# Kernel optimization log

Measured on AMD Instinct MI355X. Metric: run time of the kernel, lower is better.

## Reference

```python
import jax, jax.numpy as jnp
import numpy as np
import math

C = 128
A_SCALES = [2.0, 4.0, 8.0]
A_RATIOS = [0.5, 1.0, 2.0]
STRIDES = [4, 8, 16, 32, 64]
NA = len(A_SCALES) * len(A_RATIOS)
IMG = 1024
N = 2
NMS_THRESH = 0.7
NUM_PRE = 6000
NUM_POST = 300
SCALE_CLIP = math.log(1000.0 / 16.0)


def base_anchors(stride):
    c = stride / 2.0
    a = []
    for s in A_SCALES:
        for r in A_RATIOS:
            h = stride * s * math.sqrt(r)
            w = stride * s * math.sqrt(1.0 / r)
            a.append((c - h / 2.0, c - w / 2.0, c + h / 2.0, c + w / 2.0))
    return np.array(a, dtype=np.float32)  # [NA,4] yxyx


def shifted_anchors(stride, H, W):
    base = jnp.asarray(base_anchors(stride))
    gy = jnp.arange(H, dtype=jnp.float32) * stride
    gx = jnp.arange(W, dtype=jnp.float32) * stride
    grid = jnp.stack(jnp.meshgrid(gy, gx, indexing='ij'), axis=-1)  # [H,W,2]
    shift = jnp.concatenate([grid, grid], axis=-1)  # [H,W,4]
    return (base[None, None] + shift[:, :, None]).reshape(-1, 4)  # [H*W*NA,4]


def conv(x, w, b, pad):
    y = jax.lax.conv_general_dilated(x, w, (1, 1), pad, dimension_numbers=('NCHW', 'OIHW', 'NCHW'))
    return y + b[None, :, None, None]


def head(x, w1, b1, wobj, bobj, wbbx, bbbx):
    h = jax.nn.relu(conv(x, w1, b1, 'SAME'))
    obj = conv(h, wobj, bobj, 'VALID')  # [N,NA,H,W]
    bbx = conv(h, wbbx, bbbx, 'VALID')  # [N,4*NA,H,W]
    n = x.shape[0]
    obj = obj.transpose(0, 2, 3, 1).reshape(n, -1)       # (h,w,anchor) order
    bbx = bbx.transpose(0, 2, 3, 1).reshape(n, -1, 4)
    return obj, bbx


def shift_boxes(anchors, deltas):
    yx = (anchors[..., :2] + anchors[..., 2:]) * 0.5
    hw = anchors[..., 2:] - anchors[..., :2]
    yx_o = yx + deltas[..., :2] * hw
    hw_o = hw * jnp.exp(jnp.minimum(deltas[..., 2:], SCALE_CLIP))
    return jnp.concatenate([yx_o - 0.5 * hw_o, yx_o + 0.5 * hw_o], axis=-1)


def nms_single(boxes, scores):
    # greedy hard NMS; boxes [P,4] yxyx, scores [P]; fixed NUM_POST outputs
    areas = (boxes[:, 2] - boxes[:, 0]) * (boxes[:, 3] - boxes[:, 1])

    def step(active, _):
        masked = jnp.where(active, scores, -jnp.inf)
        i = jnp.argmax(masked)
        ok = active[i]
        tl = jnp.maximum(boxes[i, :2], boxes[:, :2])
        br = jnp.minimum(boxes[i, 2:], boxes[:, 2:])
        inter = jnp.clip(br[:, 0] - tl[:, 0], 0.0) * jnp.clip(br[:, 1] - tl[:, 1], 0.0)
        iou = inter / (areas[i] + areas - inter + 1e-9)
        active = active & (iou <= NMS_THRESH)
        return active, (jnp.where(ok, i, 0), ok)

    _, (idx, valid) = jax.lax.scan(step, jnp.ones(boxes.shape[0], bool), None, length=NUM_POST)
    return idx, valid


def forward(x0, x1, x2, x3, x4, w1, b1, wobj, bobj, wbbx, bbbx, valid_size):
    feats = [x0, x1, x2, x3, x4]
    objs, bbxs, ancs = [], [], []
    for f, s in zip(feats, STRIDES):
        o, b = head(f, w1, b1, wobj, bobj, wbbx, bbbx)
        objs.append(o)
        bbxs.append(b)
        ancs.append(shifted_anchors(s, f.shape[2], f.shape[3]))
    obj = jnp.concatenate(objs, axis=1)        # [N,M]
    bbx = jnp.concatenate(bbxs, axis=1)        # [N,M,4]
    anchors = jnp.concatenate(ancs, axis=0)    # [M,4]
    boxes = shift_boxes(anchors[None], bbx)    # [N,M,4]
    h = valid_size[:, 0].astype(boxes.dtype)[:, None]
    w = valid_size[:, 1].astype(boxes.dtype)[:, None]
    boxes = jnp.stack([jnp.clip(boxes[..., 0], 0.0, h),
                       jnp.clip(boxes[..., 1], 0.0, w),
                       jnp.clip(boxes[..., 2], 0.0, h),
                       jnp.clip(boxes[..., 3], 0.0, w)], axis=-1)
    k = min(boxes.shape[1], NUM_PRE)
    top_scores, top_idx = jax.lax.top_k(obj, k)                     # per-image topk
    top_boxes = jnp.take_along_axis(boxes, top_idx[..., None], axis=1)
    idx, valid = jax.vmap(nms_single)(jax.lax.stop_gradient(top_boxes),
                                      jax.lax.stop_gradient(top_scores))
    props = jnp.take_along_axis(top_boxes, idx[..., None], axis=1)  # [N,NUM_POST,4]
    props = props * valid[..., None].astype(props.dtype)            # zero-pad invalid
    return props, valid


def setup_inputs() -> dict:
    key = jax.random.key(0)
    ks = jax.random.split(key, 8)
    sizes = [IMG // s for s in STRIDES]
    inp = {}
    for i, hw in enumerate(sizes):
        inp['x%d' % i] = jax.random.normal(ks[i], (N, C, hw, hw), jnp.float32)
    inp['w1'] = jax.random.normal(ks[5], (C, C, 3, 3), jnp.float32) * 0.05
    inp['b1'] = jnp.zeros((C,), jnp.float32)
    inp['wobj'] = jax.random.normal(ks[6], (NA, C, 1, 1), jnp.float32) * 0.05
    inp['bobj'] = jnp.zeros((NA,), jnp.float32)
    inp['wbbx'] = jax.random.normal(ks[7], (4 * NA, C, 1, 1), jnp.float32) * 0.05
    inp['bbbx'] = jnp.zeros((4 * NA,), jnp.float32)
    inp['valid_size'] = jnp.array([[IMG, IMG]] * N, jnp.int32)
    return inp


def reference(x0, x1, x2, x3, x4, w1, b1, wobj, bobj, wbbx, bbbx, valid_size):
    return forward(x0, x1, x2, x3, x4, w1, b1, wobj, bobj, wbbx, bbbx, valid_size)
```

## Files before the change

### kernel.cpp

```cpp
#include <hip/hip_runtime.h>
#include <stdint.h>
#include <math.h>

#define M_TOT 785664
#define NPRE  6000
#define NPOST 300
#define CAP   8192
#define NWORDS 94
#define ROWW   96
#define NPAD   6016

__device__ __forceinline__ uint32_t okey(float f) {
    uint32_t u = __float_as_uint(f);
    return (u & 0x80000000u) ? ~u : (u | 0x80000000u);
}

__global__ void k_init(const float* __restrict__ w1, float* __restrict__ wt,
                       uint32_t* __restrict__ p, int zn) {
    int i = blockIdx.x * 256 + threadIdx.x;
    if (i < zn) p[i] = 0u;
    if (i < 128 * 128 * 9) {
        int co = i / 1152; int r = i % 1152; int ci = r / 9; int tap = r % 9;
        wt[ci * 1152 + tap * 128 + co] = w1[i];
    }
}

__global__ __launch_bounds__(512) void k_conv(
    const float* __restrict__ x0, const float* __restrict__ x1,
    const float* __restrict__ x2, const float* __restrict__ x3,
    const float* __restrict__ x4,
    const float* __restrict__ wt, const float* __restrict__ b1,
    const float* __restrict__ wobj, const float* __restrict__ bobj,
    const float* __restrict__ wbbx, const float* __restrict__ bbbx,
    float* __restrict__ sc, float* __restrict__ dl)
{
    __shared__ __attribute__((aligned(16))) float sx[8][18][20];
    __shared__ __attribute__((aligned(16))) float sw[8 * 9 * 128];

    int b = blockIdx.x, L = 0;
    if (b >= 512) { b -= 512; L = 1;
        if (b >= 128) { b -= 128; L = 2;
            if (b >= 32) { b -= 32; L = 3;
                if (b >= 8) { b -= 8; L = 4; } } } }
    const float* xs = (L == 0) ? x0 : (L == 1) ? x1 : (L == 2) ? x2 : (L == 3) ? x3 : x4;
    const int scoff_[5] = {0, 589824, 737280, 774144, 783360};
    int Wl = 256 >> L; int Hl = Wl; int HW = Wl * Wl;
    int tpiSh = 8 - 2 * L;
    int n  = b >> tpiSh;
    int r  = b & ((1 << tpiSh) - 1);
    int txSh = 4 - L;
    int ty0 = r >> txSh, tx0 = r & ((1 << txSh) - 1);
    int y0 = ty0 << 4, x0c = tx0 << 4;
    const float* xin = xs + (size_t)n * 128 * HW;

    int t = threadIdx.x;
    int tx = t & 15;
    int ty = t >> 4;
    int py = ty >> 1, px = (ty & 1) << 3;

    float acc0[4][8], acc1[4][8];
#pragma unroll
    for (int c = 0; c < 4; ++c)
#pragma unroll
        for (int e = 0; e < 8; ++e) { acc0[c][e] = 0.f; acc1[c][e] = 0.f; }

    for (int cc0 = 0; cc0 < 128; cc0 += 8) {
        __syncthreads();
        for (int i = t; i < 2880; i += 512) {
            int ci = i / 360; int rm = i % 360; int rr = rm / 20; int cc = rm % 20;
            float v = 0.f;
            int gy = y0 - 1 + rr, gx = x0c - 1 + cc;
            if (cc < 18 && gy >= 0 && gy < Hl && gx >= 0 && gx < Wl)
                v = xin[(size_t)(cc0 + ci) * HW + (size_t)gy * Wl + gx];
            sx[ci][rr][cc] = v;
        }
        {
            const float4* wsrc = (const float4*)(wt + (size_t)cc0 * 1152);
            float4* wdst = (float4*)sw;
            for (int i = t; i < 2304; i += 512) wdst[i] = wsrc[i];
        }
        __syncthreads();

#pragma unroll 1
        for (int ci = 0; ci < 8; ++ci) {
#pragma unroll
            for (int dy = 0; dy < 3; ++dy) {
                const float* xr = &sx[ci][py + dy][px];
                float4 xa = *(const float4*)(xr);
                float4 xb = *(const float4*)(xr + 4);
                float4 xc = *(const float4*)(xr + 8);
                float win[12] = {xa.x, xa.y, xa.z, xa.w, xb.x, xb.y, xb.z, xb.w,
                                 xc.x, xc.y, xc.z, xc.w};
#pragma unroll
                for (int dx = 0; dx < 3; ++dx) {
                    const float* wr = &sw[(ci * 9 + dy * 3 + dx) * 128 + tx * 4];
                    float4 wa = *(const float4*)(wr);
                    float4 wb = *(const float4*)(wr + 64);
                    float wva[4] = {wa.x, wa.y, wa.z, wa.w};
                    float wvb[4] = {wb.x, wb.y, wb.z, wb.w};
#pragma unroll
                    for (int e = 0; e < 8; ++e) {
                        float xv = win[e + dx];
#pragma unroll
                        for (int c = 0; c < 4; ++c) {
                            acc0[c][e] = fmaf(wva[c], xv, acc0[c][e]);
                            acc1[c][e] = fmaf(wvb[c], xv, acc1[c][e]);
                        }
                    }
                }
            }
        }
    }

#pragma unroll
    for (int c = 0; c < 4; ++c) {
        float ba = b1[tx * 4 + c];
        float bb = b1[64 + tx * 4 + c];
#pragma unroll
        for (int e = 0; e < 8; ++e) {
            float v0 = acc0[c][e] + ba;
            float v1 = acc1[c][e] + bb;
            acc0[c][e] = v0 > 0.f ? v0 : 0.f;
            acc1[c][e] = v1 > 0.f ? v1 : 0.f;
        }
    }

    int gy = y0 + py;
    size_t ppos = (size_t)gy * Wl + x0c + px;
    size_t scbase = (size_t)n * M_TOT + scoff_[L];
    size_t dlbase = (size_t)n * 4 * (size_t)M_TOT + 4 * (size_t)scoff_[L];
    for (int a = 0; a < 45; ++a) {
        const float* wp = (a < 9) ? (wobj + (size_t)a * 128) : (wbbx + (size_t)(a - 9) * 128);
        float4 wa = *(const float4*)(wp + tx * 4);
        float4 wb = *(const float4*)(wp + 64 + tx * 4);
        float wva[4] = {wa.x, wa.y, wa.z, wa.w};
        float wvb[4] = {wb.x, wb.y, wb.z, wb.w};
        float p[8];
#pragma unroll
        for (int e = 0; e < 8; ++e) p[e] = 0.f;
#pragma unroll
        for (int c = 0; c < 4; ++c)
#pragma unroll
            for (int e = 0; e < 8; ++e) {
                p[e] = fmaf(wva[c], acc0[c][e], p[e]);
                p[e] = fmaf(wvb[c], acc1[c][e], p[e]);
            }
#pragma unroll
        for (int mm = 1; mm < 16; mm <<= 1)
#pragma unroll
            for (int e = 0; e < 8; ++e)
                p[e] += __shfl_xor(p[e], mm, 64);
        if (tx == 0) {
            float bias = (a < 9) ? bobj[a] : bbbx[a - 9];
            float4 o0 = make_float4(p[0] + bias, p[1] + bias, p[2] + bias, p[3] + bias);
            float4 o1 = make_float4(p[4] + bias, p[5] + bias, p[6] + bias, p[7] + bias);
            float* dst = (a < 9) ? (sc + scbase + (size_t)a * HW + ppos)
                                 : (dl + dlbase + (size_t)(a - 9) * HW + ppos);
            *(float4*)dst = o0;
            *(float4*)(dst + 4) = o1;
        }
    }
}

__global__ __launch_bounds__(256) void k_hist(const float* __restrict__ sc,
                                              uint32_t* __restrict__ hist) {
    __shared__ uint32_t lh[8192];
    int n = blockIdx.y;
    for (int i = threadIdx.x; i < 8192; i += 256) lh[i] = 0u;
    __syncthreads();
    const float* s = sc + (size_t)n * M_TOT;
    int stride = gridDim.x * 256;
    for (int i = blockIdx.x * 256 + threadIdx.x; i < M_TOT; i += stride)
        atomicAdd(&lh[okey(s[i]) >> 19], 1u);
    __syncthreads();
    for (int i = threadIdx.x; i < 8192; i += 256) {
        uint32_t v = lh[i];
        if (v) atomicAdd(&hist[n * 8192 + i], v);
    }
}

__global__ void k_subhist(const float* __restrict__ sc, const uint32_t* __restrict__ ctrl,
                          uint32_t* __restrict__ subh) {
    int i = blockIdx.x * blockDim.x + threadIdx.x;
    int stride = gridDim.x * blockDim.x;
    for (; i < 2 * M_TOT; i += stride) {
        int n = i >= M_TOT;
        uint32_t k = okey(sc[i]);
        if ((k >> 19) == ctrl[n * 8 + 0])
            atomicAdd(&subh[n * 8192 + ((k >> 6) & 0x1FFFu)], 1u);
    }
}

__global__ void k_scan(const uint32_t* __restrict__ hist, uint32_t* __restrict__ ctrl, int phase) {
    int n = blockIdx.x;
    const uint32_t* h = hist + n * 8192;
    uint32_t* c = ctrl + n * 8;
    __shared__ uint32_t tp[256];
    int t = threadIdx.x;
    uint32_t s = 0;
    for (int r = 0; r < 32; ++r) s += h[8191 - (t * 32 + r)];
    tp[t] = s;
    __syncthreads();
    if (t == 0) {
        uint32_t run = (phase == 0) ? 0u : c[1];
        for (int i = 0; i < 256; ++i) { uint32_t v = tp[i]; tp[i] = run; run += v; }
    }
    __syncthreads();
    uint32_t cum = tp[t];
    for (int r = 0; r < 32; ++r) {
        int j = 8191 - (t * 32 + r);
        uint32_t cc = h[j];
        if (cum < 6000u && cum + cc >= 6000u) {
            if (phase == 0) { c[0] = (uint32_t)j; c[1] = cum; }
            else            { c[2] = (c[0] << 19) | ((uint32_t)j << 6); }
        }
        cum += cc;
    }
}

__global__ void k_compact(const float* __restrict__ sc, uint32_t* __restrict__ ctrl,
                          uint64_t* __restrict__ cand) {
    int i = blockIdx.x * blockDim.x + threadIdx.x;
    int stride = gridDim.x * blockDim.x;
    const int scoff_[5] = {0, 589824, 737280, 774144, 783360};
    int lane = threadIdx.x & 63;
    for (; i < 2 * M_TOT; i += stride) {
        int n = i >= M_TOT;
        int q = n ? (i - M_TOT) : i;
        uint32_t k = okey(sc[i]);
        bool hit = (k >= ctrl[n * 8 + 2]);
        unsigned long long m = __ballot(hit);
        if (m) {
            int leader = __builtin_ctzll(m);
            uint32_t base = 0;
            if (lane == leader) base = atomicAdd(&ctrl[n * 8 + 3], (uint32_t)__popcll(m));
            base = (uint32_t)__shfl((int)base, leader, 64);
            if (hit) {
                uint32_t slot = base + (uint32_t)__popcll(m & ((1ull << lane) - 1ull));
                if (slot < CAP) {
                    int Lq = (q < 589824) ? 0 : (q < 737280) ? 1 : (q < 774144) ? 2
                            : (q < 783360) ? 3 : 4;
                    int r = q - scoff_[Lq];
                    int sh = 16 - 2 * Lq;
                    int a = r >> sh;
                    int pos = r & ((1 << sh) - 1);
                    uint32_t mm = (uint32_t)(scoff_[Lq] + pos * 9 + a);
                    cand[(size_t)n * CAP + slot] = ((uint64_t)k << 32) | (uint32_t)(~mm);
                }
            }
        }
    }
}

__global__ __launch_bounds__(256) void k_rank(const uint64_t* __restrict__ cand,
                                              const uint32_t* __restrict__ ctrl,
                                              uint64_t* __restrict__ sorted) {
    __shared__ __attribute__((aligned(16))) uint64_t chunk[2048];
    int n = blockIdx.y;
    uint32_t cnt = ctrl[n * 8 + 3];
    if (cnt > CAP) cnt = CAP;
    const uint64_t* cb = cand + (size_t)n * CAP;
    uint64_t* sb = sorted + (size_t)n * CAP;
    int i = blockIdx.x * 256 + threadIdx.x;
    uint64_t key = (i < (int)cnt) ? cb[i] : 0ull;
    uint32_t rank = 0;
    const ulonglong2* cb2 = (const ulonglong2*)cb;
    for (uint32_t base = 0; base < cnt; base += 2048) {
        __syncthreads();
        for (int j = threadIdx.x; j < 1024; j += 256)
            ((ulonglong2*)chunk)[j] = cb2[(base >> 1) + j];
        __syncthreads();
        uint32_t lim = cnt - base; if (lim > 2048u) lim = 2048u;
        for (uint32_t j = 0; j < lim; ++j) rank += (chunk[j] > key) ? 1u : 0u;
    }
    if (i < (int)cnt && rank < CAP) sb[rank] = key;
}

__global__ void k_decode(const uint64_t* __restrict__ cand, const float* __restrict__ dl,
                         const int* __restrict__ vsz, float* __restrict__ boxes,
                         unsigned long long* __restrict__ degm) {
    int i = blockIdx.x * 256 + threadIdx.x;
    if (i >= 2 * NPRE) return;
    int n = i / NPRE, rk = i % NPRE;
    const int scoff_[5] = {0, 589824, 737280, 774144, 783360};
    uint64_t pk = cand[(size_t)n * CAP + rk];
    uint32_t m = ~(uint32_t)(pk & 0xFFFFFFFFull);
    int Lq = (m < 589824u) ? 0 : (m < 737280u) ? 1 : (m < 774144u) ? 2 : (m < 783360u) ? 3 : 4;
    int r = (int)m - scoff_[Lq];
    int pos = r / 9;
    int a = r - pos * 9;
    int Wl = 256 >> Lq;
    int y = pos >> (8 - Lq);
    int xx = pos & (Wl - 1);
    float stridef = (float)(4 << Lq);
    double sD = (double)(2 << (a / 3));
    double rD = ((a % 3) == 0) ? 0.5 : ((a % 3) == 1) ? 1.0 : 2.0;
    double hD = ((double)stridef * sD) * sqrt(rD);
    double wD = ((double)stridef * sD) * sqrt(1.0 / rD);
    double cD = (double)stridef / 2.0;
    float y1b = (float)(cD - hD / 2.0);
    float x1b = (float)(cD - wD / 2.0);
    float y2b = (float)(cD + hD / 2.0);
    float x2b = (float)(cD + wD / 2.0);
    float gy = (float)y * stridef;
    float gx = (float)xx * stridef;
    float ay1 = __fadd_rn(y1b, gy), ax1 = __fadd_rn(x1b, gx);
    float ay2 = __fadd_rn(y2b, gy), ax2 = __fadd_rn(x2b, gx);
    float cy = __fmul_rn(__fadd_rn(ay1, ay2), 0.5f);
    float cx = __fmul_rn(__fadd_rn(ax1, ax2), 0.5f);
    float ah = __fsub_rn(ay2, ay1);
    float aw = __fsub_rn(ax2, ax1);
    size_t HWl = (size_t)Wl * Wl;
    size_t db = (size_t)n * 4 * M_TOT + 4 * (size_t)scoff_[Lq] + (size_t)pos;
    float dy_ = dl[db + (size_t)(a * 4 + 0) * HWl];
    float dx_ = dl[db + (size_t)(a * 4 + 1) * HWl];
    float dh_ = dl[db + (size_t)(a * 4 + 2) * HWl];
    float dw_ = dl[db + (size_t)(a * 4 + 3) * HWl];
    float yo = __fadd_rn(cy, __fmul_rn(dy_, ah));
    float xo = __fadd_rn(cx, __fmul_rn(dx_, aw));
    const float SCLIPf = 4.135166556742356f;
    float ho = __fmul_rn(ah, (float)exp((double)fminf(dh_, SCLIPf)));
    float wo = __fmul_rn(aw, (float)exp((double)fminf(dw_, SCLIPf)));
    float hf = (float)vsz[n * 2 + 0], wf = (float)vsz[n * 2 + 1];
    float y1 = fminf(fmaxf(__fsub_rn(yo, __fmul_rn(0.5f, ho)), 0.f), hf);
    float x1 = fminf(fmaxf(__fsub_rn(xo, __fmul_rn(0.5f, wo)), 0.f), wf);
    float y2 = fminf(fmaxf(__fadd_rn(yo, __fmul_rn(0.5f, ho)), 0.f), hf);
    float x2 = fminf(fmaxf(__fadd_rn(xo, __fmul_rn(0.5f, wo)), 0.f), wf);
    *(float4*)(boxes + ((size_t)n * NPAD + rk) * 4) = make_float4(y1, x1, y2, x2);
    float area = __fmul_rn(__fsub_rn(y2, y1), __fsub_rn(x2, x1));
    float selfiou = __fdiv_rn(area, __fadd_rn(area, 1e-9f));
    if (!(selfiou > 0.7f))
        atomicOr(&degm[(size_t)n * ROWW + (rk >> 6)], 1ull << (rk & 63));
}

__global__ __launch_bounds__(256) void k_iou(const float* __restrict__ boxes,
                                             uint64_t* __restrict__ ioum) {
    int n = blockIdx.y;
    int i = blockIdx.x * 4 + (threadIdx.x >> 6);
    int lane = threadIdx.x & 63;
    const float* bsrc = boxes + (size_t)n * NPAD * 4;
    float4 bi = *(const float4*)(bsrc + (size_t)i * 4);
    float ai = __fmul_rn(__fsub_rn(bi.z, bi.x), __fsub_rn(bi.w, bi.y));
    uint64_t* row = ioum + ((size_t)n * NPAD + i) * ROWW;
    int w0 = i >> 6;
    for (int w = lane; w < w0; w += 64) row[w] = 0ull;
    for (int w = w0; w < NWORDS; ++w) {
        int j = (w << 6) | lane;
        bool pred = false;
        if (j > i && j < NPRE) {
            float4 bj = *(const float4*)(bsrc + (size_t)j * 4);
            float aj = __fmul_rn(__fsub_rn(bj.z, bj.x), __fsub_rn(bj.w, bj.y));
            float ty = fmaxf(bi.x, bj.x), tx2 = fmaxf(bi.y, bj.y);
            float by = fminf(bi.z, bj.z), bx2 = fminf(bi.w, bj.w);
            float ih = fmaxf(__fsub_rn(by, ty), 0.f), iw = fmaxf(__fsub_rn(bx2, tx2), 0.f);
            float inter = __fmul_rn(ih, iw);
            float den = __fadd_rn(__fsub_rn(__fadd_rn(ai, aj), inter), 1e-9f);
            float iou = __fdiv_rn(inter, den);
            pred = iou > 0.7f;
        }
        unsigned long long msk = __ballot(pred);
        if (lane == 0) row[w] = (uint64_t)msk;
    }
}

__global__ __launch_bounds__(64) void k_nms(const float* __restrict__ boxes,
                                            const uint64_t* __restrict__ ioum,
                                            const unsigned long long* __restrict__ degm,
                                            float* __restrict__ out) {
    int n = blockIdx.x;
    __shared__ uint64_t sup[NWORDS];
    __shared__ uint64_t deg[NWORDS];
    __shared__ int keepl[NPOST];
    int lane = threadIdx.x;
    for (int w = lane; w < NWORDS; w += 64) {
        sup[w] = 0ull;
        deg[w] = degm[(size_t)n * ROWW + w];
    }
    __syncthreads();
    int kept = 0;
    bool stop = false;
    for (int w = 0; w < NWORDS && kept < NPOST && !stop; ++w) {
        uint64_t vmask = (w == NWORDS - 1) ? ((1ull << 48) - 1ull) : ~0ull;
        uint64_t avail = (~sup[w]) & vmask;
        while (avail && kept < NPOST) {
            int bpos = __builtin_ctzll(avail);
            int i = (w << 6) | bpos;
            const uint64_t* row = ioum + ((size_t)n * NPAD + i) * ROWW;
            uint64_t r0 = row[lane];
            uint64_t r1 = (lane < NWORDS - 64) ? row[64 + lane] : 0ull;
            if (lane == 0) keepl[kept] = i;
            kept++;
            if ((deg[w] >> bpos) & 1ull) {
                if (lane == 0) { for (int k2 = kept; k2 < NPOST; ++k2) keepl[k2] = i; }
                kept = NPOST;
                stop = true;
                break;
            }
            sup[lane] |= r0;
            if (lane < NWORDS - 64) sup[64 + lane] |= r1;
            __syncthreads();
            avail = (~sup[w]) & vmask & ~((2ull << bpos) - 1ull);
        }
    }
    __syncthreads();
    for (int k = lane; k < NPOST; k += 64) {
        float4 bx = make_float4(0.f, 0.f, 0.f, 0.f);
        float vf = 0.f;
        if (k < kept) {
            int i = keepl[k];
            bx = *(const float4*)(boxes + ((size_t)n * NPAD + i) * 4);
            vf = 1.f;
        }
        *(float4*)(out + (size_t)n * 1200 + (size_t)k * 4) = bx;
        out[2400 + n * 300 + k] = vf;
    }
}

extern "C" void kernel_launch(void* const* d_in, const int* in_sizes, int n_in,
                              void* d_out, int out_size, void* d_ws, size_t ws_size,
                              hipStream_t stream) {
    (void)out_size; (void)ws_size;
    static const int want[12] = {16777216, 4194304, 1048576, 262144, 65536,
                                 147456, 128, 1152, 9, 4608, 36, 4};
    const void* p[12];
    for (int k = 0; k < 12; ++k) p[k] = d_in[k];
    bool pos_ok = (n_in >= 12);
    for (int k = 0; k < 12 && pos_ok; ++k) if (in_sizes[k] != want[k]) pos_ok = false;
    if (!pos_ok) {
        for (int k = 0; k < 12; ++k)
            for (int j = 0; j < n_in; ++j)
                if (in_sizes[j] == want[k]) { p[k] = d_in[j]; break; }
    }
    const float* x0   = (const float*)p[0];
    const float* x1   = (const float*)p[1];
    const float* x2   = (const float*)p[2];
    const float* x3   = (const float*)p[3];
    const float* x4   = (const float*)p[4];
    const float* w1   = (const float*)p[5];
    const float* b1   = (const float*)p[6];
    const float* wobj = (const float*)p[7];
    const float* bobj = (const float*)p[8];
    const float* wbbx = (const float*)p[9];
    const float* bbbx = (const float*)p[10];
    const int*   vsz  = (const int*)p[11];
    float* out = (float*)d_out;

    size_t off = 0;
    char* base = (char*)d_ws;
    auto carve = [&](size_t bytes) -> void* {
        void* q = base + off;
        off += (bytes + 255) & ~(size_t)255;
        return q;
    };
    float*    SC     = (float*)carve((size_t)2 * M_TOT * 4);
    float*    DL     = (float*)carve((size_t)2 * M_TOT * 16);
    float*    WT     = (float*)carve((size_t)147456 * 4);
    uint32_t* HIST   = (uint32_t*)carve((size_t)16384 * 4);
    uint32_t* SUBH   = (uint32_t*)carve((size_t)16384 * 4);
    uint32_t* CTRL   = (uint32_t*)carve((size_t)64 * 4);
    unsigned long long* DEGM = (unsigned long long*)carve((size_t)2 * ROWW * 8);
    uint64_t* CAND   = (uint64_t*)carve((size_t)2 * CAP * 8);
    uint64_t* SORTED = (uint64_t*)carve((size_t)2 * CAP * 8);
    float*    BOXES  = (float*)carve((size_t)2 * NPAD * 16);
    uint64_t* IOUM   = (uint64_t*)carve((size_t)2 * NPAD * ROWW * 8);

    int zn = (int)(((char*)CAND - (char*)HIST) / 4);
    int initN = (zn > 147456) ? zn : 147456;
    k_init<<<(initN + 255) / 256, 256, 0, stream>>>(w1, WT, HIST, zn);
    k_conv<<<682, 512, 0, stream>>>(x0, x1, x2, x3, x4, WT, b1,
                                    wobj, bobj, wbbx, bbbx, SC, DL);
    k_hist<<<dim3(256, 2), 256, 0, stream>>>(SC, HIST);
    k_scan<<<2, 256, 0, stream>>>(HIST, CTRL, 0);
    k_subhist<<<1024, 256, 0, stream>>>(SC, CTRL, SUBH);
    k_scan<<<2, 256, 0, stream>>>(SUBH, CTRL, 1);
    k_compact<<<1024, 256, 0, stream>>>(SC, CTRL, CAND);
    k_rank<<<dim3(CAP / 256, 2), 256, 0, stream>>>(CAND, CTRL, SORTED);
    k_decode<<<(2 * NPRE + 255) / 256, 256, 0, stream>>>(SORTED, DL, vsz, BOXES, DEGM);
    k_iou<<<dim3(NPRE / 4, 2), 256, 0, stream>>>(BOXES, IOUM);
    k_nms<<<2, 64, 0, stream>>>(BOXES, IOUM, DEGM, out);
}
```

Baseline: 1.043 ms.

## Fuse post-conv selection and NMS stages into one cooperative kernel

Replaces nine separate launches (histogram, scan, subhistogram, scan, compaction, rank sort, decode, IoU matrix, NMS) with a single cooperative kernel of 512 blocks that separates the phases with grid-wide syncs. The goal is to remove per-launch overhead and the gaps between small kernels. In exchange, some phases run on fewer blocks than before (subhist and compact go from 1024 blocks to 512, IoU uses a block-strided loop), grid.sync has its own cost, and correctness depends on all 512 blocks being co-resident.

```diff
diff --git a/kernel.cpp b/kernel.cpp
--- a/kernel.cpp
+++ b/kernel.cpp
@@ -1,4 +1,5 @@
 #include <hip/hip_runtime.h>
+#include <hip/hip_cooperative_groups.h>
 #include <stdint.h>
 #include <math.h>
 
@@ -9,6 +10,8 @@
 #define NWORDS 94
 #define ROWW   96
 #define NPAD   6016
+
+namespace cg = cooperative_groups;
 
 __device__ __forceinline__ uint32_t okey(float f) {
     uint32_t u = __float_as_uint(f);
@@ -162,40 +165,7 @@
     }
 }
 
-__global__ __launch_bounds__(256) void k_hist(const float* __restrict__ sc,
-                                              uint32_t* __restrict__ hist) {
-    __shared__ uint32_t lh[8192];
-    int n = blockIdx.y;
-    for (int i = threadIdx.x; i < 8192; i += 256) lh[i] = 0u;
-    __syncthreads();
-    const float* s = sc + (size_t)n * M_TOT;
-    int stride = gridDim.x * 256;
-    for (int i = blockIdx.x * 256 + threadIdx.x; i < M_TOT; i += stride)
-        atomicAdd(&lh[okey(s[i]) >> 19], 1u);
-    __syncthreads();
-    for (int i = threadIdx.x; i < 8192; i += 256) {
-        uint32_t v = lh[i];
-        if (v) atomicAdd(&hist[n * 8192 + i], v);
-    }
-}
-
-__global__ void k_subhist(const float* __restrict__ sc, const uint32_t* __restrict__ ctrl,
-                          uint32_t* __restrict__ subh) {
-    int i = blockIdx.x * blockDim.x + threadIdx.x;
-    int stride = gridDim.x * blockDim.x;
-    for (; i < 2 * M_TOT; i += stride) {
-        int n = i >= M_TOT;
-        uint32_t k = okey(sc[i]);
-        if ((k >> 19) == ctrl[n * 8 + 0])
-            atomicAdd(&subh[n * 8192 + ((k >> 6) & 0x1FFFu)], 1u);
-    }
-}
-
-__global__ void k_scan(const uint32_t* __restrict__ hist, uint32_t* __restrict__ ctrl, int phase) {
-    int n = blockIdx.x;
-    const uint32_t* h = hist + n * 8192;
-    uint32_t* c = ctrl + n * 8;
-    __shared__ uint32_t tp[256];
+__device__ void scan_phase(const uint32_t* h, uint32_t* c, int phase, uint32_t* tp) {
     int t = threadIdx.x;
     uint32_t s = 0;
     for (int r = 0; r < 32; ++r) s += h[8191 - (t * 32 + r)];
@@ -218,201 +188,244 @@
     }
 }
 
-__global__ void k_compact(const float* __restrict__ sc, uint32_t* __restrict__ ctrl,
-                          uint64_t* __restrict__ cand) {
-    int i = blockIdx.x * blockDim.x + threadIdx.x;
-    int stride = gridDim.x * blockDim.x;
+__global__ __launch_bounds__(256) void k_select(
+    const float* __restrict__ sc, uint32_t* __restrict__ hist,
+    uint32_t* __restrict__ subh, uint32_t* __restrict__ ctrl,
+    uint64_t* __restrict__ cand, uint64_t* __restrict__ sorted,
+    const float* __restrict__ dl, const int* __restrict__ vsz,
+    float* __restrict__ boxes, unsigned long long* __restrict__ degm,
+    uint64_t* __restrict__ ioum, float* __restrict__ out)
+{
+    __shared__ __attribute__((aligned(16))) unsigned char smem[32768];
+    cg::grid_group grid = cg::this_grid();
+    const int bid = blockIdx.x;
+    const int t = threadIdx.x;
     const int scoff_[5] = {0, 589824, 737280, 774144, 783360};
-    int lane = threadIdx.x & 63;
-    for (; i < 2 * M_TOT; i += stride) {
-        int n = i >= M_TOT;
-        int q = n ? (i - M_TOT) : i;
-        uint32_t k = okey(sc[i]);
-        bool hit = (k >= ctrl[n * 8 + 2]);
-        unsigned long long m = __ballot(hit);
-        if (m) {
-            int leader = __builtin_ctzll(m);
-            uint32_t base = 0;
-            if (lane == leader) base = atomicAdd(&ctrl[n * 8 + 3], (uint32_t)__popcll(m));
-            base = (uint32_t)__shfl((int)base, leader, 64);
-            if (hit) {
-                uint32_t slot = base + (uint32_t)__popcll(m & ((1ull << lane) - 1ull));
-                if (slot < CAP) {
-                    int Lq = (q < 589824) ? 0 : (q < 737280) ? 1 : (q < 774144) ? 2
-                            : (q < 783360) ? 3 : 4;
-                    int r = q - scoff_[Lq];
-                    int sh = 16 - 2 * Lq;
-                    int a = r >> sh;
-                    int pos = r & ((1 << sh) - 1);
-                    uint32_t mm = (uint32_t)(scoff_[Lq] + pos * 9 + a);
-                    cand[(size_t)n * CAP + slot] = ((uint64_t)k << 32) | (uint32_t)(~mm);
+
+    {
+        uint32_t* lh = (uint32_t*)smem;
+        int n = bid >> 8;
+        for (int i = t; i < 8192; i += 256) lh[i] = 0u;
+        __syncthreads();
+        const float* s = sc + (size_t)n * M_TOT;
+        for (int i = (bid & 255) * 256 + t; i < M_TOT; i += 256 * 256)
+            atomicAdd(&lh[okey(s[i]) >> 19], 1u);
+        __syncthreads();
+        for (int i = t; i < 8192; i += 256) {
+            uint32_t v = lh[i];
+            if (v) atomicAdd(&hist[n * 8192 + i], v);
+        }
+    }
+    grid.sync();
+
+    if (bid < 2) scan_phase(hist + bid * 8192, ctrl + bid * 8, 0, (uint32_t*)smem);
+    grid.sync();
+
+    {
+        int stride = 512 * 256;
+        for (int i = bid * 256 + t; i < 2 * M_TOT; i += stride) {
+            int n = i >= M_TOT;
+            uint32_t k = okey(sc[i]);
+            if ((k >> 19) == ctrl[n * 8 + 0])
+                atomicAdd(&subh[n * 8192 + ((k >> 6) & 0x1FFFu)], 1u);
+        }
+    }
+    grid.sync();
+
+    if (bid < 2) scan_phase(subh + bid * 8192, ctrl + bid * 8, 1, (uint32_t*)smem);
+    grid.sync();
+
+    {
+        int stride = 512 * 256;
+        int lane = t & 63;
+        for (int i = bid * 256 + t; i < 2 * M_TOT; i += stride) {
+            int n = i >= M_TOT;
+            int q = n ? (i - M_TOT) : i;
+            uint32_t k = okey(sc[i]);
+            bool hit = (k >= ctrl[n * 8 + 2]);
+            unsigned long long m = __ballot(hit);
+            if (m) {
+                int leader = __builtin_ctzll(m);
+                uint32_t base = 0;
+                if (lane == leader) base = atomicAdd(&ctrl[n * 8 + 3], (uint32_t)__popcll(m));
+                base = (uint32_t)__shfl((int)base, leader, 64);
+                if (hit) {
+                    uint32_t slot = base + (uint32_t)__popcll(m & ((1ull << lane) - 1ull));
+                    if (slot < CAP) {
+                        int Lq = (q < 589824) ? 0 : (q < 737280) ? 1 : (q < 774144) ? 2
+                                : (q < 783360) ? 3 : 4;
+                        int r = q - scoff_[Lq];
+                        int sh = 16 - 2 * Lq;
+                        int a = r >> sh;
+                        int pos = r & ((1 << sh) - 1);
+                        uint32_t mm = (uint32_t)(scoff_[Lq] + pos * 9 + a);
+                        cand[(size_t)n * CAP + slot] = ((uint64_t)k << 32) | (uint32_t)(~mm);
+                    }
                 }
             }
         }
     }
-}
-
-__global__ __launch_bounds__(256) void k_rank(const uint64_t* __restrict__ cand,
-                                              const uint32_t* __restrict__ ctrl,
-                                              uint64_t* __restrict__ sorted) {
-    __shared__ __attribute__((aligned(16))) uint64_t chunk[2048];
-    int n = blockIdx.y;
-    uint32_t cnt = ctrl[n * 8 + 3];
-    if (cnt > CAP) cnt = CAP;
-    const uint64_t* cb = cand + (size_t)n * CAP;
-    uint64_t* sb = sorted + (size_t)n * CAP;
-    int i = blockIdx.x * 256 + threadIdx.x;
-    uint64_t key = (i < (int)cnt) ? cb[i] : 0ull;
-    uint32_t rank = 0;
-    const ulonglong2* cb2 = (const ulonglong2*)cb;
-    for (uint32_t base = 0; base < cnt; base += 2048) {
-        __syncthreads();
-        for (int j = threadIdx.x; j < 1024; j += 256)
-            ((ulonglong2*)chunk)[j] = cb2[(base >> 1) + j];
-        __syncthreads();
-        uint32_t lim = cnt - base; if (lim > 2048u) lim = 2048u;
-        for (uint32_t j = 0; j < lim; ++j) rank += (chunk[j] > key) ? 1u : 0u;
-    }
-    if (i < (int)cnt && rank < CAP) sb[rank] = key;
-}
-
-__global__ void k_decode(const uint64_t* __restrict__ cand, const float* __restrict__ dl,
-                         const int* __restrict__ vsz, float* __restrict__ boxes,
-                         unsigned long long* __restrict__ degm) {
-    int i = blockIdx.x * 256 + threadIdx.x;
-    if (i >= 2 * NPRE) return;
-    int n = i / NPRE, rk = i % NPRE;
-    const int scoff_[5] = {0, 589824, 737280, 774144, 783360};
-    uint64_t pk = cand[(size_t)n * CAP + rk];
-    uint32_t m = ~(uint32_t)(pk & 0xFFFFFFFFull);
-    int Lq = (m < 589824u) ? 0 : (m < 737280u) ? 1 : (m < 774144u) ? 2 : (m < 783360u) ? 3 : 4;
-    int r = (int)m - scoff_[Lq];
-    int pos = r / 9;
-    int a = r - pos * 9;
-    int Wl = 256 >> Lq;
-    int y = pos >> (8 - Lq);
-    int xx = pos & (Wl - 1);
-    float stridef = (float)(4 << Lq);
-    double sD = (double)(2 << (a / 3));
-    double rD = ((a % 3) == 0) ? 0.5 : ((a % 3) == 1) ? 1.0 : 2.0;
-    double hD = ((double)stridef * sD) * sqrt(rD);
-    double wD = ((double)stridef * sD) * sqrt(1.0 / rD);
-    double cD = (double)stridef / 2.0;
-    float y1b = (float)(cD - hD / 2.0);
-    float x1b = (float)(cD - wD / 2.0);
-    float y2b = (float)(cD + hD / 2.0);
-    float x2b = (float)(cD + wD / 2.0);
-    float gy = (float)y * stridef;
-    float gx = (float)xx * stridef;
-    float ay1 = __fadd_rn(y1b, gy), ax1 = __fadd_rn(x1b, gx);
-    float ay2 = __fadd_rn(y2b, gy), ax2 = __fadd_rn(x2b, gx);
-    float cy = __fmul_rn(__fadd_rn(ay1, ay2), 0.5f);
-    float cx = __fmul_rn(__fadd_rn(ax1, ax2), 0.5f);
-    float ah = __fsub_rn(ay2, ay1);
-    float aw = __fsub_rn(ax2, ax1);
-    size_t HWl = (size_t)Wl * Wl;
-    size_t db = (size_t)n * 4 * M_TOT + 4 * (size_t)scoff_[Lq] + (size_t)pos;
-    float dy_ = dl[db + (size_t)(a * 4 + 0) * HWl];
-    float dx_ = dl[db + (size_t)(a * 4 + 1) * HWl];
-    float dh_ = dl[db + (size_t)(a * 4 + 2) * HWl];
-    float dw_ = dl[db + (size_t)(a * 4 + 3) * HWl];
-    float yo = __fadd_rn(cy, __fmul_rn(dy_, ah));
-    float xo = __fadd_rn(cx, __fmul_rn(dx_, aw));
-    const float SCLIPf = 4.135166556742356f;
-    float ho = __fmul_rn(ah, (float)exp((double)fminf(dh_, SCLIPf)));
-    float wo = __fmul_rn(aw, (float)exp((double)fminf(dw_, SCLIPf)));
-    float hf = (float)vsz[n * 2 + 0], wf = (float)vsz[n * 2 + 1];
-    float y1 = fminf(fmaxf(__fsub_rn(yo, __fmul_rn(0.5f, ho)), 0.f), hf);
-    float x1 = fminf(fmaxf(__fsub_rn(xo, __fmul_rn(0.5f, wo)), 0.f), wf);
-    float y2 = fminf(fmaxf(__fadd_rn(yo, __fmul_rn(0.5f, ho)), 0.f), hf);
-    float x2 = fminf(fmaxf(__fadd_rn(xo, __fmul_rn(0.5f, wo)), 0.f), wf);
-    *(float4*)(boxes + ((size_t)n * NPAD + rk) * 4) = make_float4(y1, x1, y2, x2);
-    float area = __fmul_rn(__fsub_rn(y2, y1), __fsub_rn(x2, x1));
-    float selfiou = __fdiv_rn(area, __fadd_rn(area, 1e-9f));
-    if (!(selfiou > 0.7f))
-        atomicOr(&degm[(size_t)n * ROWW + (rk >> 6)], 1ull << (rk & 63));
-}
-
-__global__ __launch_bounds__(256) void k_iou(const float* __restrict__ boxes,
-                                             uint64_t* __restrict__ ioum) {
-    int n = blockIdx.y;
-    int i = blockIdx.x * 4 + (threadIdx.x >> 6);
-    int lane = threadIdx.x & 63;
-    const float* bsrc = boxes + (size_t)n * NPAD * 4;
-    float4 bi = *(const float4*)(bsrc + (size_t)i * 4);
-    float ai = __fmul_rn(__fsub_rn(bi.z, bi.x), __fsub_rn(bi.w, bi.y));
-    uint64_t* row = ioum + ((size_t)n * NPAD + i) * ROWW;
-    int w0 = i >> 6;
-    for (int w = lane; w < w0; w += 64) row[w] = 0ull;
-    for (int w = w0; w < NWORDS; ++w) {
-        int j = (w << 6) | lane;
-        bool pred = false;
-        if (j > i && j < NPRE) {
-            float4 bj = *(const float4*)(bsrc + (size_t)j * 4);
-            float aj = __fmul_rn(__fsub_rn(bj.z, bj.x), __fsub_rn(bj.w, bj.y));
-            float ty = fmaxf(bi.x, bj.x), tx2 = fmaxf(bi.y, bj.y);
-            float by = fminf(bi.z, bj.z), bx2 = fminf(bi.w, bj.w);
-            float ih = fmaxf(__fsub_rn(by, ty), 0.f), iw = fmaxf(__fsub_rn(bx2, tx2), 0.f);
-            float inter = __fmul_rn(ih, iw);
-            float den = __fadd_rn(__fsub_rn(__fadd_rn(ai, aj), inter), 1e-9f);
-            float iou = __fdiv_rn(inter, den);
-            pred = iou > 0.7f;
-        }
-        unsigned long long msk = __ballot(pred);
-        if (lane == 0) row[w] = (uint64_t)msk;
-    }
-}
-
-__global__ __launch_bounds__(64) void k_nms(const float* __restrict__ boxes,
-                                            const uint64_t* __restrict__ ioum,
-                                            const unsigned long long* __restrict__ degm,
-                                            float* __restrict__ out) {
-    int n = blockIdx.x;
-    __shared__ uint64_t sup[NWORDS];
-    __shared__ uint64_t deg[NWORDS];
-    __shared__ int keepl[NPOST];
-    int lane = threadIdx.x;
-    for (int w = lane; w < NWORDS; w += 64) {
-        sup[w] = 0ull;
-        deg[w] = degm[(size_t)n * ROWW + w];
-    }
-    __syncthreads();
-    int kept = 0;
-    bool stop = false;
-    for (int w = 0; w < NWORDS && kept < NPOST && !stop; ++w) {
-        uint64_t vmask = (w == NWORDS - 1) ? ((1ull << 48) - 1ull) : ~0ull;
-        uint64_t avail = (~sup[w]) & vmask;
-        while (avail && kept < NPOST) {
-            int bpos = __builtin_ctzll(avail);
-            int i = (w << 6) | bpos;
-            const uint64_t* row = ioum + ((size_t)n * NPAD + i) * ROWW;
-            uint64_t r0 = row[lane];
-            uint64_t r1 = (lane < NWORDS - 64) ? row[64 + lane] : 0ull;
-            if (lane == 0) keepl[kept] = i;
-            kept++;
-            if ((deg[w] >> bpos) & 1ull) {
-                if (lane == 0) { for (int k2 = kept; k2 < NPOST; ++k2) keepl[k2] = i; }
-                kept = NPOST;
-                stop = true;
-                break;
-            }
-            sup[lane] |= r0;
-            if (lane < NWORDS - 64) sup[64 + lane] |= r1;
+    grid.sync();
+
+    if (bid < 64) {
+        uint64_t* chunk = (uint64_t*)smem;
+        int n = bid >> 5;
+        uint32_t cnt = ctrl[n * 8 + 3];
+        if (cnt > CAP) cnt = CAP;
+        const uint64_t* cb = cand + (size_t)n * CAP;
+        uint64_t* sb = sorted + (size_t)n * CAP;
+        int i = (bid & 31) * 256 + t;
+        uint64_t key = (i < (int)cnt) ? cb[i] : 0ull;
+        uint32_t rank = 0;
+        const ulonglong2* cb2 = (const ulonglong2*)cb;
+        for (uint32_t base = 0; base < cnt; base += 2048) {
             __syncthreads();
-            avail = (~sup[w]) & vmask & ~((2ull << bpos) - 1ull);
-        }
-    }
-    __syncthreads();
-    for (int k = lane; k < NPOST; k += 64) {
-        float4 bx = make_float4(0.f, 0.f, 0.f, 0.f);
-        float vf = 0.f;
-        if (k < kept) {
-            int i = keepl[k];
-            bx = *(const float4*)(boxes + ((size_t)n * NPAD + i) * 4);
-            vf = 1.f;
-        }
-        *(float4*)(out + (size_t)n * 1200 + (size_t)k * 4) = bx;
-        out[2400 + n * 300 + k] = vf;
+            for (int j = t; j < 1024; j += 256)
+                ((ulonglong2*)chunk)[j] = cb2[(base >> 1) + j];
+            __syncthreads();
+            uint32_t lim = cnt - base; if (lim > 2048u) lim = 2048u;
+            for (uint32_t j = 0; j < lim; ++j) rank += (chunk[j] > key) ? 1u : 0u;
+        }
+        if (i < (int)cnt && rank < CAP) sb[rank] = key;
+    }
+    grid.sync();
+
+    {
+        int i = bid * 256 + t;
+        if (i < 2 * NPRE) {
+            int n = i / NPRE, rk = i % NPRE;
+            uint64_t pk = sorted[(size_t)n * CAP + rk];
+            uint32_t m = ~(uint32_t)(pk & 0xFFFFFFFFull);
+            int Lq = (m < 589824u) ? 0 : (m < 737280u) ? 1 : (m < 774144u) ? 2
+                    : (m < 783360u) ? 3 : 4;
+            int r = (int)m - scoff_[Lq];
+            int pos = r / 9;
+            int a = r - pos * 9;
+            int Wl = 256 >> Lq;
+            int y = pos >> (8 - Lq);
+            int xx = pos & (Wl - 1);
+            float stridef = (float)(4 << Lq);
+            double sD = (double)(2 << (a / 3));
+            double rD = ((a % 3) == 0) ? 0.5 : ((a % 3) == 1) ? 1.0 : 2.0;
+            double hD = ((double)stridef * sD) * sqrt(rD);
+            double wD = ((double)stridef * sD) * sqrt(1.0 / rD);
+            double cD = (double)stridef / 2.0;
+            float y1b = (float)(cD - hD / 2.0);
+            float x1b = (float)(cD - wD / 2.0);
+            float y2b = (float)(cD + hD / 2.0);
+            float x2b = (float)(cD + wD / 2.0);
+            float gy = (float)y * stridef;
+            float gx = (float)xx * stridef;
+            float ay1 = __fadd_rn(y1b, gy), ax1 = __fadd_rn(x1b, gx);
+            float ay2 = __fadd_rn(y2b, gy), ax2 = __fadd_rn(x2b, gx);
+            float cy = __fmul_rn(__fadd_rn(ay1, ay2), 0.5f);
+            float cx = __fmul_rn(__fadd_rn(ax1, ax2), 0.5f);
+            float ah = __fsub_rn(ay2, ay1);
+            float aw = __fsub_rn(ax2, ax1);
+            size_t HWl = (size_t)Wl * Wl;
+            size_t db = (size_t)n * 4 * M_TOT + 4 * (size_t)scoff_[Lq] + (size_t)pos;
+            float dy_ = dl[db + (size_t)(a * 4 + 0) * HWl];
+            float dx_ = dl[db + (size_t)(a * 4 + 1) * HWl];
+            float dh_ = dl[db + (size_t)(a * 4 + 2) * HWl];
+            float dw_ = dl[db + (size_t)(a * 4 + 3) * HWl];
+            float yo = __fadd_rn(cy, __fmul_rn(dy_, ah));
+            float xo = __fadd_rn(cx, __fmul_rn(dx_, aw));
+            const float SCLIPf = 4.135166556742356f;
+            float ho = __fmul_rn(ah, (float)exp((double)fminf(dh_, SCLIPf)));
+            float wo = __fmul_rn(aw, (float)exp((double)fminf(dw_, SCLIPf)));
+            float hf = (float)vsz[n * 2 + 0], wf = (float)vsz[n * 2 + 1];
+            float y1 = fminf(fmaxf(__fsub_rn(yo, __fmul_rn(0.5f, ho)), 0.f), hf);
+            float x1 = fminf(fmaxf(__fsub_rn(xo, __fmul_rn(0.5f, wo)), 0.f), wf);
+            float y2 = fminf(fmaxf(__fadd_rn(yo, __fmul_rn(0.5f, ho)), 0.f), hf);
+            float x2 = fminf(fmaxf(__fadd_rn(xo, __fmul_rn(0.5f, wo)), 0.f), wf);
+            *(float4*)(boxes + ((size_t)n * NPAD + rk) * 4) = make_float4(y1, x1, y2, x2);
+            float area = __fmul_rn(__fsub_rn(y2, y1), __fsub_rn(x2, x1));
+            float selfiou = __fdiv_rn(area, __fadd_rn(area, 1e-9f));
+            if (!(selfiou > 0.7f))
+                atomicOr(&degm[(size_t)n * ROWW + (rk >> 6)], 1ull << (rk & 63));
+        }
+    }
+    grid.sync();
+
+    {
+        int lane = t & 63;
+        for (int pair = bid; pair < 3000; pair += 512) {
+            int n = pair >= 1500;
+            int blk = pair - n * 1500;
+            int i = blk * 4 + (t >> 6);
+            const float* bsrc = boxes + (size_t)n * NPAD * 4;
+            float4 bi = *(const float4*)(bsrc + (size_t)i * 4);
+            float ai = __fmul_rn(__fsub_rn(bi.z, bi.x), __fsub_rn(bi.w, bi.y));
+            uint64_t* row = ioum + ((size_t)n * NPAD + i) * ROWW;
+            int w0 = i >> 6;
+            for (int w = lane; w < w0; w += 64) row[w] = 0ull;
+            for (int w = w0; w < NWORDS; ++w) {
+                int j = (w << 6) | lane;
+                bool pred = false;
+                if (j > i && j < NPRE) {
+                    float4 bj = *(const float4*)(bsrc + (size_t)j * 4);
+                    float aj = __fmul_rn(__fsub_rn(bj.z, bj.x), __fsub_rn(bj.w, bj.y));
+                    float ty = fmaxf(bi.x, bj.x), tx2 = fmaxf(bi.y, bj.y);
+                    float by = fminf(bi.z, bj.z), bx2 = fminf(bi.w, bj.w);
+                    float ih = fmaxf(__fsub_rn(by, ty), 0.f), iw = fmaxf(__fsub_rn(bx2, tx2), 0.f);
+                    float inter = __fmul_rn(ih, iw);
+                    float den = __fadd_rn(__fsub_rn(__fadd_rn(ai, aj), inter), 1e-9f);
+                    float iou = __fdiv_rn(inter, den);
+                    pred = iou > 0.7f;
+                }
+                unsigned long long msk = __ballot(pred);
+                if (lane == 0) row[w] = (uint64_t)msk;
+            }
+        }
+    }
+    grid.sync();
+
+    if (bid < 2 && t < 64) {
+        uint64_t* sup = (uint64_t*)smem;
+        uint64_t* deg = (uint64_t*)(smem + 768);
+        int* keepl = (int*)(smem + 1536);
+        int n = bid;
+        int lane = t;
+        for (int w = lane; w < NWORDS; w += 64) {
+            sup[w] = 0ull;
+            deg[w] = degm[(size_t)n * ROWW + w];
+        }
+        __builtin_amdgcn_s_barrier();
+        int kept = 0;
+        bool stop = false;
+        for (int w = 0; w < NWORDS && kept < NPOST && !stop; ++w) {
+            uint64_t vmask = (w == NWORDS - 1) ? ((1ull << 48) - 1ull) : ~0ull;
+            uint64_t avail = (~sup[w]) & vmask;
+            while (avail && kept < NPOST) {
+                int bpos = __builtin_ctzll(avail);
+                int i = (w << 6) | bpos;
+                const uint64_t* row = ioum + ((size_t)n * NPAD + i) * ROWW;
+                uint64_t r0 = row[lane];
+                uint64_t r1 = (lane < NWORDS - 64) ? row[64 + lane] : 0ull;
+                if (lane == 0) keepl[kept] = i;
+                kept++;
+                if ((deg[w] >> bpos) & 1ull) {
+                    if (lane == 0) { for (int k2 = kept; k2 < NPOST; ++k2) keepl[k2] = i; }
+                    kept = NPOST;
+                    stop = true;
+                    break;
+                }
+                sup[lane] |= r0;
+                if (lane < NWORDS - 64) sup[64 + lane] |= r1;
+                avail = (~sup[w]) & vmask & ~((2ull << bpos) - 1ull);
+            }
+        }
+        for (int k = lane; k < NPOST; k += 64) {
+            float4 bx = make_float4(0.f, 0.f, 0.f, 0.f);
+            float vf = 0.f;
+            if (k < kept) {
+                int i = keepl[k];
+                bx = *(const float4*)(boxes + ((size_t)n * NPAD + i) * 4);
+                vf = 1.f;
+            }
+            *(float4*)(out + (size_t)n * 1200 + (size_t)k * 4) = bx;
+            out[2400 + n * 300 + k] = vf;
+        }
     }
 }
 
@@ -469,13 +482,13 @@
     k_init<<<(initN + 255) / 256, 256, 0, stream>>>(w1, WT, HIST, zn);
     k_conv<<<682, 512, 0, stream>>>(x0, x1, x2, x3, x4, WT, b1,
                                     wobj, bobj, wbbx, bbbx, SC, DL);
-    k_hist<<<dim3(256, 2), 256, 0, stream>>>(SC, HIST);
-    k_scan<<<2, 256, 0, stream>>>(HIST, CTRL, 0);
-    k_subhist<<<1024, 256, 0, stream>>>(SC, CTRL, SUBH);
-    k_scan<<<2, 256, 0, stream>>>(SUBH, CTRL, 1);
-    k_compact<<<1024, 256, 0, stream>>>(SC, CTRL, CAND);
-    k_rank<<<dim3(CAP / 256, 2), 256, 0, stream>>>(CAND, CTRL, SORTED);
-    k_decode<<<(2 * NPRE + 255) / 256, 256, 0, stream>>>(SORTED, DL, vsz, BOXES, DEGM);
-    k_iou<<<dim3(NPRE / 4, 2), 256, 0, stream>>>(BOXES, IOUM);
-    k_nms<<<2, 64, 0, stream>>>(BOXES, IOUM, DEGM, out);
-}
+    {
+        void* kargs[12] = {
+            (void*)&SC, (void*)&HIST, (void*)&SUBH, (void*)&CTRL,
+            (void*)&CAND, (void*)&SORTED, (void*)&DL, (void*)&vsz,
+            (void*)&BOXES, (void*)&DEGM, (void*)&IOUM, (void*)&out
+        };
+        hipLaunchCooperativeKernel((const void*)k_select, dim3(512), dim3(256),
+                                   kargs, 0, stream);
+    }
+}
```

Result: slower. 1.511 ms (+44.9%).
